# Performance work log

Hardware: AMD Instinct MI355X
Metric: run time of the kernel (lower is better)

Reference implementation:

```python
import jax, jax.numpy as jnp
import numpy as np


def setup_inputs() -> dict:
    key = jax.random.key(0)
    k1, k2, k3, k4, k5 = jax.random.split(key, 5)
    B, T, N, F, H = 32, 12, 512, 64, 64
    cat_x = jax.random.normal(k1, (B, T, N, F), dtype=jnp.float32)
    # Linear params (stored as [in, out]; torch stores [out, in] and does x @ W.T)
    lim = 1.0 / np.sqrt(F)
    Wq = jax.random.uniform(k2, (F, H), jnp.float32, -lim, lim)
    bq = jax.random.uniform(k3, (H,), jnp.float32, -lim, lim)
    Wk = jax.random.uniform(k4, (F, H), jnp.float32, -lim, lim)
    bk = jax.random.uniform(k5, (H,), jnp.float32, -lim, lim)
    return {"cat_x": cat_x, "Wq": Wq, "bq": bq, "Wk": Wk, "bk": bk, "tau": 4}


def reference(cat_x, Wq, bq, Wk, bk, tau):
    # cat_x: [B, T, N, F]
    q = cat_x @ Wq + bq  # [B, T, N, H]
    k = cat_x @ Wk + bk  # [B, T, N, H]
    qf = jnp.fft.rfft(q, axis=-1)  # [B, T, N, Fr]
    kf = jnp.fft.rfft(k, axis=-1)  # [B, T, N, Fr]
    # Vectorized over the original Python loop over i (query time step):
    # res[b, i, j, n, :] = qf[b, i, n, :] * conj(kf[b, j, n, :])
    res = qf[:, :, None, :, :] * jnp.conj(kf)[:, None, :, :, :]  # [B, Ti, Tj, N, Fr]
    corr = jnp.fft.irfft(res, axis=-1)  # [B, Ti, Tj, N, H] (H even -> exact round trip)
    # mean over batch, then hidden (last), then nodes == mean over (B, N, H)
    score_set = jnp.mean(corr, axis=(0, 3, 4))  # [Ti, Tj]
    scores, indices = jax.lax.top_k(score_set, tau)
    return scores, indices
```

## Files before the change

kernel.cpp:

```cpp
#include <hip/hip_runtime.h>

#define BB 32
#define TT 12
#define NN 512
#define FF 64
#define HH 64
#define NBLK 64

__global__ __launch_bounds__(256) void fft_sel_main(
    const float* __restrict__ x,
    const float* __restrict__ Wq,
    const float* __restrict__ bq,
    const float* __restrict__ Wk,
    const float* __restrict__ bk,
    float* __restrict__ S)
{
    __shared__ float wq_s[FF];
    __shared__ float wk_s[FF];
    __shared__ float bsum[2];
    __shared__ float sq[TT][NBLK];
    __shared__ float sk[TT][NBLK];

    const int tid = threadIdx.x;

    if (tid < FF) {
        float a = 0.f;
        #pragma unroll
        for (int h = 0; h < HH; ++h) a += Wq[tid * HH + h];
        wq_s[tid] = a;
    } else if (tid < 2 * FF) {
        const int f = tid - FF;
        float a = 0.f;
        #pragma unroll
        for (int h = 0; h < HH; ++h) a += Wk[f * HH + h];
        wk_s[f] = a;
    } else if (tid == 2 * FF) {
        float a = 0.f;
        #pragma unroll
        for (int h = 0; h < HH; ++h) a += bq[h];
        bsum[0] = a;
    } else if (tid == 2 * FF + 1) {
        float a = 0.f;
        #pragma unroll
        for (int h = 0; h < HH; ++h) a += bk[h];
        bsum[1] = a;
    }
    __syncthreads();

    const int b  = blockIdx.x >> 3;
    const int n0 = (blockIdx.x & 7) * NBLK;
    const float bqs = bsum[0];
    const float bks = bsum[1];

    for (int r = tid; r < TT * NBLK; r += 256) {
        const int t  = r >> 6;
        const int nl = r & 63;
        const float4* xp = (const float4*)(x +
            (((size_t)b * TT + t) * NN + (n0 + nl)) * FF);
        float dq = 0.f, dk = 0.f;
        #pragma unroll
        for (int u = 0; u < FF / 4; ++u) {
            const float4 v = xp[u];
            dq += v.x * wq_s[4*u]   + v.y * wq_s[4*u+1]
                + v.z * wq_s[4*u+2] + v.w * wq_s[4*u+3];
            dk += v.x * wk_s[4*u]   + v.y * wk_s[4*u+1]
                + v.z * wk_s[4*u+2] + v.w * wk_s[4*u+3];
        }
        sq[t][nl] = dq + bqs;
        sk[t][nl] = dk + bks;
    }
    __syncthreads();

    if (tid < TT * TT) {
        const int i = tid / TT;
        const int j = tid % TT;
        float acc = 0.f;
        #pragma unroll
        for (int nl = 0; nl < NBLK; ++nl) acc += sq[i][nl] * sk[j][nl];
        atomicAdd(&S[tid], acc);
    }
}

__global__ void fft_sel_final(const float* __restrict__ S, float* __restrict__ out)
{
    const int i = threadIdx.x;
    if (i >= TT) return;
    const float scale = 1.0f / ((float)BB * (float)NN * (float)HH);
    float v[TT];
    bool used[TT];
    #pragma unroll
    for (int j = 0; j < TT; ++j) { v[j] = S[i * TT + j] * scale; used[j] = false; }
    #pragma unroll
    for (int s = 0; s < 4; ++s) {
        float best = -INFINITY;
        int bi = 0;
        for (int j = 0; j < TT; ++j) {
            if (!used[j] && v[j] > best) { best = v[j]; bi = j; }
        }
        used[bi] = true;
        out[i * 4 + s]            = best;
        out[TT * 4 + i * 4 + s]   = (float)bi;
    }
}

extern "C" void kernel_launch(void* const* d_in, const int* in_sizes, int n_in,
                              void* d_out, int out_size, void* d_ws, size_t ws_size,
                              hipStream_t stream) {
    const float* x  = (const float*)d_in[0];
    const float* Wq = (const float*)d_in[1];
    const float* bq = (const float*)d_in[2];
    const float* Wk = (const float*)d_in[3];
    const float* bk = (const float*)d_in[4];
    float* S = (float*)d_ws;

    hipMemsetAsync(d_ws, 0, TT * TT * sizeof(float), stream);
    fft_sel_main<<<BB * (NN / NBLK), 256, 0, stream>>>(x, Wq, bq, Wk, bk, S);
    fft_sel_final<<<1, 64, 0, stream>>>(S, (float*)d_out);
}
```

Before: 99.63 us.

## Coalesce x loads with 16-lane dot products and precompute weight sums once

Moves the Wq/Wk/bias column sums out of every block into a single init kernel that also zeroes the accumulator, which replaces the memset. The main kernel now has 16 lanes cooperatively load one row of x as contiguous float4s and reduce with shuffles, instead of each thread striding through a whole row. Block size over nodes is halved, doubling the grid and the number of atomics. Shared arrays are padded. The aim is coalesced loads of the 50MB input and no redundant per-block weight reduction, at the cost of extra shuffle work and an extra launch.

```diff
diff --git a/kernel.cpp b/kernel.cpp
--- a/kernel.cpp
+++ b/kernel.cpp
@@ -5,69 +5,89 @@
 #define NN 512
 #define FF 64
 #define HH 64
-#define NBLK 64
+#define NBLK 32
+#define NCHUNK (NN / NBLK)
+#define GRID (BB * NCHUNK)
+
+#define WS_S  0
+#define WS_WQ 144
+#define WS_WK 208
+#define WS_BQ 272
+#define WS_BK 273
+
+__global__ __launch_bounds__(384) void fft_sel_init(
+    const float* __restrict__ Wq, const float* __restrict__ bq,
+    const float* __restrict__ Wk, const float* __restrict__ bk,
+    float* __restrict__ ws)
+{
+    const int tid = threadIdx.x;
+    if (tid < TT * TT) {
+        ws[WS_S + tid] = 0.f;
+    } else if (tid >= 144 && tid < 144 + FF) {
+        const int f = tid - 144;
+        float a = 0.f;
+        #pragma unroll
+        for (int h = 0; h < HH; ++h) a += Wq[f * HH + h];
+        ws[WS_WQ + f] = a;
+    } else if (tid >= 208 && tid < 208 + FF) {
+        const int f = tid - 208;
+        float a = 0.f;
+        #pragma unroll
+        for (int h = 0; h < HH; ++h) a += Wk[f * HH + h];
+        ws[WS_WK + f] = a;
+    } else if (tid == 272) {
+        float a = 0.f;
+        #pragma unroll
+        for (int h = 0; h < HH; ++h) a += bq[h];
+        ws[WS_BQ] = a;
+    } else if (tid == 273) {
+        float a = 0.f;
+        #pragma unroll
+        for (int h = 0; h < HH; ++h) a += bk[h];
+        ws[WS_BK] = a;
+    }
+}
 
 __global__ __launch_bounds__(256) void fft_sel_main(
     const float* __restrict__ x,
-    const float* __restrict__ Wq,
-    const float* __restrict__ bq,
-    const float* __restrict__ Wk,
-    const float* __restrict__ bk,
+    const float* __restrict__ ws,
     float* __restrict__ S)
 {
-    __shared__ float wq_s[FF];
-    __shared__ float wk_s[FF];
-    __shared__ float bsum[2];
-    __shared__ float sq[TT][NBLK];
-    __shared__ float sk[TT][NBLK];
+    __shared__ float sq[TT][NBLK + 1];
+    __shared__ float sk[TT][NBLK + 1];
 
-    const int tid = threadIdx.x;
+    const int tid  = threadIdx.x;
+    const int wave = tid >> 6;
+    const int lane = tid & 63;
+    const int sub  = lane >> 4;
+    const int q    = lane & 15;
 
-    if (tid < FF) {
-        float a = 0.f;
+    const float4 wqv = *(const float4*)(ws + WS_WQ + 4 * q);
+    const float4 wkv = *(const float4*)(ws + WS_WK + 4 * q);
+    const float  bqs = ws[WS_BQ];
+    const float  bks = ws[WS_BK];
+
+    const int b  = blockIdx.x >> 4;
+    const int n0 = (blockIdx.x & (NCHUNK - 1)) * NBLK;
+
+    #pragma unroll
+    for (int it = 0; it < (TT * NBLK) / 16; ++it) {
+        const int r  = it * 16 + wave * 4 + sub;
+        const int t  = r >> 5;
+        const int nl = r & (NBLK - 1);
+        const float4 v = *(const float4*)(x +
+            (((size_t)b * TT + t) * NN + (n0 + nl)) * FF + q * 4);
+        float pq = v.x * wqv.x + v.y * wqv.y + v.z * wqv.z + v.w * wqv.w;
+        float pk = v.x * wkv.x + v.y * wkv.y + v.z * wkv.z + v.w * wkv.w;
         #pragma unroll
-        for (int h = 0; h < HH; ++h) a += Wq[tid * HH + h];
-        wq_s[tid] = a;
-    } else if (tid < 2 * FF) {
-        const int f = tid - FF;
-        float a = 0.f;
-        #pragma unroll
-        for (int h = 0; h < HH; ++h) a += Wk[f * HH + h];
-        wk_s[f] = a;
-    } else if (tid == 2 * FF) {
-        float a = 0.f;
-        #pragma unroll
-        for (int h = 0; h < HH; ++h) a += bq[h];
-        bsum[0] = a;
-    } else if (tid == 2 * FF + 1) {
-        float a = 0.f;
-        #pragma unroll
-        for (int h = 0; h < HH; ++h) a += bk[h];
-        bsum[1] = a;
-    }
-    __syncthreads();
-
-    const int b  = blockIdx.x >> 3;
-    const int n0 = (blockIdx.x & 7) * NBLK;
-    const float bqs = bsum[0];
-    const float bks = bsum[1];
-
-    for (int r = tid; r < TT * NBLK; r += 256) {
-        const int t  = r >> 6;
-        const int nl = r & 63;
-        const float4* xp = (const float4*)(x +
-            (((size_t)b * TT + t) * NN + (n0 + nl)) * FF);
-        float dq = 0.f, dk = 0.f;
-        #pragma unroll
-        for (int u = 0; u < FF / 4; ++u) {
-            const float4 v = xp[u];
-            dq += v.x * wq_s[4*u]   + v.y * wq_s[4*u+1]
-                + v.z * wq_s[4*u+2] + v.w * wq_s[4*u+3];
-            dk += v.x * wk_s[4*u]   + v.y * wk_s[4*u+1]
-                + v.z * wk_s[4*u+2] + v.w * wk_s[4*u+3];
+        for (int off = 1; off < 16; off <<= 1) {
+            pq += __shfl_xor(pq, off);
+            pk += __shfl_xor(pk, off);
         }
-        sq[t][nl] = dq + bqs;
-        sk[t][nl] = dk + bks;
+        if (q == 0) {
+            sq[t][nl] = pq + bqs;
+            sk[t][nl] = pk + bks;
+        }
     }
     __syncthreads();
 
@@ -98,8 +118,8 @@
             if (!used[j] && v[j] > best) { best = v[j]; bi = j; }
         }
         used[bi] = true;
-        out[i * 4 + s]            = best;
-        out[TT * 4 + i * 4 + s]   = (float)bi;
+        out[i * 4 + s]          = best;
+        out[TT * 4 + i * 4 + s] = (float)bi;
     }
 }
 
@@ -111,9 +131,9 @@
     const float* bq = (const float*)d_in[2];
     const float* Wk = (const float*)d_in[3];
     const float* bk = (const float*)d_in[4];
-    float* S = (float*)d_ws;
+    float* ws = (float*)d_ws;
 
-    hipMemsetAsync(d_ws, 0, TT * TT * sizeof(float), stream);
-    fft_sel_main<<<BB * (NN / NBLK), 256, 0, stream>>>(x, Wq, bq, Wk, bk, S);
-    fft_sel_final<<<1, 64, 0, stream>>>(S, (float*)d_out);
+    fft_sel_init<<<1, 384, 0, stream>>>(Wq, bq, Wk, bk, ws);
+    fft_sel_main<<<GRID, 256, 0, stream>>>(x, ws, ws + WS_S);
+    fft_sel_final<<<1, 64, 0, stream>>>(ws + WS_S, (float*)d_out);
 }
```

New measurement: 109.6 us. 1.1x slower.
